# Kernel optimization log

Measured on AMD Instinct MI355X. Metric: run time of the kernel, lower is better.

The kernel has to match this reference:

```python
import jax, jax.numpy as jnp
import numpy as np

NUM_NODES = 100
WINDOW = 128
GH = 256       # graph_hidden_channels
DH = 64        # discrepancy_hidden_channels
OUT = 128      # out_channels
B = 256        # graphs per batch
N = B * NUM_NODES
E = 409600


def _mconv(x, w, b):
    # x: [B, n, W], w: [n, 2, k], b: [n, 2]  (per-node Conv1d(1,2,k), 'same' padding)
    k = w.shape[-1]
    W = x.shape[-1]
    p = k // 2
    xp = jnp.pad(x, ((0, 0), (0, 0), (p, p)))
    win = jnp.stack([xp[..., j:j + W] for j in range(k)], axis=-1)  # [B,n,W,k]
    return jnp.einsum('bnwk,nck->bncw', win, w) + b[None, :, :, None]


def _gcn(x, edge_index, Wg, bg):
    # PyG GCNConv: add self-loops, symmetric normalization, then linear
    Nn = x.shape[0]
    xw = x @ Wg.T
    loops = jnp.arange(Nn, dtype=edge_index.dtype)
    src = jnp.concatenate([edge_index[0], loops])
    dst = jnp.concatenate([edge_index[1], loops])
    deg = jax.ops.segment_sum(jnp.ones(src.shape[0], dtype=xw.dtype), dst, num_segments=Nn)
    norm = jax.lax.rsqrt(jnp.maximum(deg, 1e-12))
    coef = norm[src] * norm[dst]
    agg = jax.ops.segment_sum(coef[:, None] * xw[src], dst, num_segments=Nn)
    return agg + bg


def setup_inputs() -> dict:
    key = jax.random.key(0)
    ks = jax.random.split(key, 20)
    f = 6 * WINDOW
    s = lambda d: 1.0 / np.sqrt(d)
    inp = {
        'x1': jax.random.normal(ks[0], (N, WINDOW), jnp.float32),
        'x2': jax.random.normal(ks[1], (N, WINDOW), jnp.float32),
        'edge_index1': jax.random.randint(ks[2], (2, E), 0, N, jnp.int32),
        'edge_index2': jax.random.randint(ks[3], (2, E), 0, N, jnp.int32),
        'w3': jax.random.normal(ks[4], (NUM_NODES, 2, 3), jnp.float32) * s(3),
        'b3': jax.random.normal(ks[5], (NUM_NODES, 2), jnp.float32) * s(3),
        'w5': jax.random.normal(ks[6], (NUM_NODES, 2, 5), jnp.float32) * s(5),
        'b5': jax.random.normal(ks[7], (NUM_NODES, 2), jnp.float32) * s(5),
        'w7': jax.random.normal(ks[8], (NUM_NODES, 2, 7), jnp.float32) * s(7),
        'b7': jax.random.normal(ks[9], (NUM_NODES, 2), jnp.float32) * s(7),
        'Wff': jax.random.normal(ks[10], (NUM_NODES, GH, f), jnp.float32) * s(f),
        'bff': jax.random.normal(ks[11], (NUM_NODES, GH), jnp.float32) * s(f),
        'Wg': jax.random.normal(ks[12], (GH, GH), jnp.float32) * s(GH),
        'bg': jax.random.normal(ks[13], (GH,), jnp.float32) * s(GH),
        'Wd': jax.random.normal(ks[14], (NUM_NODES, DH, 2 * GH), jnp.float32) * s(2 * GH),
        'bd': jax.random.normal(ks[15], (NUM_NODES, DH), jnp.float32) * s(2 * GH),
        'Wfc': jax.random.normal(ks[16], (OUT, NUM_NODES * DH), jnp.float32) * s(NUM_NODES * DH),
        'bfc': jax.random.normal(ks[17], (OUT,), jnp.float32) * s(NUM_NODES * DH),
    }
    return inp


def reference(x1, x2, edge_index1, edge_index2, w3, b3, w5, b5, w7, b7,
              Wff, bff, Wg, bg, Wd, bd, Wfc, bfc):
    n = w3.shape[0]
    Nn, W = x1.shape
    Bg = Nn // n

    def branch(x):
        xg = x.reshape(Bg, n, W)
        # multiscale CNN: concat conv3/conv5/conv7 along channel -> [B,n,6,W]
        c = jnp.concatenate([_mconv(xg, w3, b3), _mconv(xg, w5, b5), _mconv(xg, w7, b7)], axis=2)
        c = jax.nn.relu(c.reshape(Bg, n, 6 * W))            # channel-major flatten (matches view(-1))
        h = jax.nn.relu(jnp.einsum('bnf,nhf->bnh', c, Wff) + bff)
        return h.reshape(Nn, -1)

    h1 = jax.nn.relu(_gcn(branch(x1), edge_index1, Wg, bg))
    h2 = jax.nn.relu(_gcn(branch(x2), edge_index2, Wg, bg))
    H = h1.shape[-1]
    cat = jnp.concatenate([h1.reshape(Bg, n, H), h2.reshape(Bg, n, H)], axis=-1)  # [B,n,2H]
    d = jnp.einsum('bnf,ndf->bnd', cat, Wd) + bd            # per-node discrepancy FC
    du = jax.nn.relu(d.reshape(Bg, -1))                     # node-major -> [B, n*DH]
    return du @ Wfc.T + bfc
```

## Files before the change

kernel.cpp:

```cpp
#include <hip/hip_runtime.h>

#define DI __device__ __forceinline__

typedef __bf16 bf16_t;
typedef bf16_t bf16x8 __attribute__((ext_vector_type(8)));
typedef float f32x4 __attribute__((ext_vector_type(4)));
typedef ushort ushort8v __attribute__((ext_vector_type(8)));

static constexpr int NNODE = 100, WIN = 128, GH = 256, DH = 64, OUTC = 128, NB = 256;
static constexpr int NTOT = NB * NNODE;
static constexpr int NE = 409600;
static constexpr int FFK = 6 * WIN;
static constexpr size_t CB = (size_t)NNODE * NB * FFK;
static constexpr size_t HB = (size_t)NTOT * GH;
static constexpr int CVT_BLKS = 23264;
static constexpr int NSEG = 64, SEGE = NE / NSEG;
static constexpr int NPK = NTOT / 2;
static constexpr int NRANGE = 4, RDST = NTOT / NRANGE;
static constexpr int RPK = RDST / 2;
static constexpr int HIST_BLKS = 2 * NSEG * NRANGE;

DI ushort f2bf(float f) {
  union { float f; unsigned u; } v; v.f = f;
  unsigned r = v.u + 0x7fffu + ((v.u >> 16) & 1u);
  return (ushort)(r >> 16);
}
DI float bf2f(ushort s) {
  union { unsigned u; float f; } v; v.u = ((unsigned)s) << 16; return v.f;
}
DI float u2f(uint u) { union { uint u; float f; } v; v.u = u; return v.f; }

DI void gload16(const void* g, void* l) {
  __builtin_amdgcn_global_load_lds((const __attribute__((address_space(1))) void*)g,
                                   (__attribute__((address_space(3))) void*)l, 16, 0, 0);
}


DI void cvt_body(int bx, const float* s0, const float* s1, const float* s2, const float* s3,
                 ushort* d0, ushort* d1, ushort* d2, ushort* d3) {
  int j = bx * 256 + threadIdx.x;
  const float* s; ushort* d;
  if (j < 19660800 / 4) { s = s0; d = d0; }
  else if ((j -= 19660800 / 4) < 3276800 / 4) { s = s1; d = d1; }
  else if ((j -= 3276800 / 4) < 819200 / 4) { s = s2; d = d2; }
  else { j -= 819200 / 4; s = s3; d = d3; }
  float4 v = reinterpret_cast<const float4*>(s)[j];
  ushort4 o;
  o.x = f2bf(v.x); o.y = f2bf(v.y); o.z = f2bf(v.z); o.w = f2bf(v.w);
  reinterpret_cast<ushort4*>(d)[j] = o;
}

DI void histseg_body(int bx, const int* e1d, const int* e2d,
                     ushort* rank_local, uint* segcnt, uint* cnt ) {
  int set = bx & 1, seg = (bx >> 1) & (NSEG - 1), range = bx >> 7;
  int tid = threadIdx.x;
  for (int k = tid; k < RPK; k += 256) cnt[k] = 0;
  __syncthreads();
  const int* dstp = (set ? e2d : e1d) + seg * SEGE;
  ushort* rl = rank_local + set * NE + seg * SEGE;
  const int dbase = range * RDST;
#pragma unroll
  for (int k = 0; k < SEGE / 256; ++k) {
    int i = k * 256 + tid;
    uint dl = (uint)(dstp[i] - dbase);
    if (dl < (uint)RDST) {
      uint sh = (dl & 1) * 16;
      uint old = atomicAdd(&cnt[dl >> 1], 1u << sh);
      rl[i] = (ushort)((old >> sh) & 0xffffu);
    }
  }
  __syncthreads();
  uint* sc = segcnt + (size_t)(set * NSEG + seg) * NPK + range * RPK;
  for (int k = tid; k < RPK; k += 256) sc[k] = cnt[k];
}

DI void fill_body(int bx, const int* e1, const int* e2, const int* offs,
                  const ushort* rank_local, const uint* segbase, int* csr) {
  int i = bx * 256 + threadIdx.x;
  int set = i >= NE;
  int ii = i - set * NE;
  const int* e = set ? e2 : e1;
  int d = e[NE + ii];
  int seg = ii / SEGE;
  uint b32 = segbase[(size_t)(set * NSEG + seg) * NPK + (d >> 1)];
  int base = (b32 >> ((d & 1) * 16)) & 0xffff;
  int pos = offs[set * (NTOT + 1) + d] + base + rank_local[i];
  csr[set * NE + pos] = e[ii];
}

DI void segscan_body(int set, int pb, const uint* segcnt, uint* segbase, int* deg) {
  int p = pb * 256 + threadIdx.x;
  uint lo = 0, hi = 0;
  const uint* sc = segcnt + (size_t)set * NSEG * NPK + p;
  uint* sb = segbase + (size_t)set * NSEG * NPK + p;
  for (int s = 0; s < NSEG; ++s) {
    uint v = sc[(size_t)s * NPK];
    sb[(size_t)s * NPK] = lo | (hi << 16);
    lo += v & 0xffffu; hi += v >> 16;
  }
  reinterpret_cast<int2*>(deg)[set * NPK + p] = make_int2((int)lo, (int)hi);
}

DI void scan_body(int set, const int* deg_, int* offs_, float* norm_) {
  const int* deg = deg_ + set * NTOT;
  int* offs = offs_ + set * (NTOT + 1);
  float* norm = norm_ + set * NTOT;
  __shared__ int part[256];
  int t = threadIdx.x;
  int base = t * 100;
  int s = 0;
  for (int j = 0; j < 100; ++j) s += deg[base + j];
  part[t] = s;
  __syncthreads();
  for (int d = 1; d < 256; d <<= 1) {
    int vv = (t >= d) ? part[t - d] : 0;
    __syncthreads();
    part[t] += vv;
    __syncthreads();
  }
  int run = (t > 0) ? part[t - 1] : 0;
  for (int j = 0; j < 100; ++j) {
    int dv = deg[base + j];
    offs[base + j] = run;
    norm[base + j] = rsqrtf((float)(dv + 1));
    run += dv;
  }
  if (t == 255) offs[NTOT] = part[255];
}

DI void conv_body(int bx, const float* x1, const float* x2,
                  const float* w3, const float* b3, const float* w5, const float* b5,
                  const float* w7, const float* b7, ushort* c, float* xs ) {
  const int t = threadIdx.x;
  const int rowi = t >> 4;
  const int idx = t & 15;
  int r = bx * 16 + rowi;
  int br = r >= NTOT;
  int rr = r - br * NTOT;
  const float* x = br ? x2 : x1;
  int b = rr / 100, node = rr - b * 100;

  float* row = xs + rowi * 136;
  const int w0 = idx * 8;
  float4 v0 = *reinterpret_cast<const float4*>(x + (size_t)rr * WIN + w0);
  float4 v1 = *reinterpret_cast<const float4*>(x + (size_t)rr * WIN + w0 + 4);
  *reinterpret_cast<float4*>(&row[4 + w0]) = v0;
  *reinterpret_cast<float4*>(&row[4 + w0 + 4]) = v1;
  if (idx == 0) { row[0] = 0.f; row[1] = 0.f; row[2] = 0.f; row[3] = 0.f; }
  if (idx == 15) { row[132] = 0.f; row[133] = 0.f; row[134] = 0.f; row[135] = 0.f; }
  __syncthreads();

  float xv[14];
#pragma unroll
  for (int j = 0; j < 14; ++j) xv[j] = row[1 + w0 + j];

  const float* W3 = w3 + node * 6;  const float* B3 = b3 + node * 2;
  const float* W5 = w5 + node * 10; const float* B5 = b5 + node * 2;
  const float* W7 = w7 + node * 14; const float* B7 = b7 + node * 2;
  ushort* out = c + (size_t)br * CB + (size_t)(node * NB + b) * FFK + w0;

#pragma unroll
  for (int ch = 0; ch < 2; ++ch) {
    float k3[3], k5[5], k7[7];
#pragma unroll
    for (int j = 0; j < 3; ++j) k3[j] = W3[ch * 3 + j];
#pragma unroll
    for (int j = 0; j < 5; ++j) k5[j] = W5[ch * 5 + j];
#pragma unroll
    for (int j = 0; j < 7; ++j) k7[j] = W7[ch * 7 + j];
    float bb3 = B3[ch], bb5 = B5[ch], bb7 = B7[ch];
    ushort8v o3, o5, o7;
#pragma unroll
    for (int p = 0; p < 8; ++p) {
      float a3 = bb3, a5 = bb5, a7 = bb7;
#pragma unroll
      for (int j = 0; j < 3; ++j) a3 += k3[j] * xv[p + 2 + j];
#pragma unroll
      for (int j = 0; j < 5; ++j) a5 += k5[j] * xv[p + 1 + j];
#pragma unroll
      for (int j = 0; j < 7; ++j) a7 += k7[j] * xv[p + j];
      o3[p] = f2bf(fmaxf(a3, 0.f));
      o5[p] = f2bf(fmaxf(a5, 0.f));
      o7[p] = f2bf(fmaxf(a7, 0.f));
    }
    *reinterpret_cast<ushort8v*>(out + (0 + ch) * WIN) = o3;
    *reinterpret_cast<ushort8v*>(out + (2 + ch) * WIN) = o5;
    *reinterpret_cast<ushort8v*>(out + (4 + ch) * WIN) = o7;
  }
}

template <int MODE>
DI void gemm_body(int bx, int by, const ushort* __restrict__ A, const ushort* __restrict__ A2,
                  const ushort* __restrict__ Bm, ushort* __restrict__ obf,
                  float* __restrict__ of, const float* __restrict__ bias) {
  constexpr int BN = (MODE == 2 || MODE == 0) ? 64 : 128;
  constexpr int KT = (MODE == 0) ? 12 : (MODE == 1) ? 4 : (MODE == 2) ? 8 : 4;
  constexpr int LDA = (MODE == 0) ? 768 : (MODE == 1) ? 256 : (MODE == 2) ? 256 : 6400;
  constexpr int LDB = (MODE == 0) ? 768 : (MODE == 1) ? 256 : (MODE == 2) ? 512 : 6400;
  constexpr int MF = (MODE == 2) ? 2 : 4;
  constexpr int NF = (MODE == 0) ? 2 : 4;
  constexpr int NTW = (MODE == 0) ? 64 : 128;

  __shared__ ushort As[128 * 64];
  __shared__ ushort Bs[BN * 64];

  const int tid = threadIdx.x, wv = tid >> 6, lane = tid & 63;
  const int j8 = (((lane & 7) ^ (lane >> 3)) - (lane & 7)) * 8;

  int mt = 0, nt = 0, node = 0, kbase = 0, br = 0;
  if constexpr (MODE == 0) {
    int h = bx;
    int s = (h & 7) * 200 + (h >> 3);
    nt = s & 3; int rest = s >> 2;
    mt = rest & 1; int yy = rest >> 1;
    br = yy >= 100; node = yy - br * 100;
  } else if constexpr (MODE == 1) {
    int h = bx;
    int s = (h & 7) * 100 + (h >> 3);
    nt = s & 1; int rest = s >> 1;
    br = rest >= 200; mt = rest - br * 200;
  } else if constexpr (MODE == 2) { mt = bx; node = by; }
  else { mt = bx; kbase = by * 256; }

  const ushort* Ab = nullptr; const ushort* Bb = nullptr;
  if constexpr (MODE == 0) { Ab = A + (size_t)br * CB + (size_t)node * (NB * FFK) + (size_t)mt * 128 * FFK;
                             Bb = Bm + (size_t)node * (GH * FFK) + (size_t)nt * 64 * FFK; }
  else if constexpr (MODE == 1) { Ab = A + (size_t)br * HB + (size_t)mt * 128 * GH;
                                  Bb = Bm + (size_t)nt * 128 * GH; }
  else if constexpr (MODE == 2) { Bb = Bm + (size_t)node * (DH * 512); }
  else { Ab = A + (size_t)mt * 128 * 6400 + kbase; Bb = Bm + kbase; }

  const int wr = (MODE == 2) ? wv : (wv >> 1);
  const int wc = (MODE == 2) ? 0 : (wv & 1);

  f32x4 acc[MF][NF] = {};

  for (int kt = 0; kt < KT; ++kt) {
    const int k0 = kt * 64;
    __syncthreads();
#pragma unroll
    for (int it = 0; it < 4; ++it) {
      int rb = it * 32 + wv * 8;
      int row = rb + (lane >> 3);
      const ushort* gp;
      if constexpr (MODE == 2) {
        int b_ = mt * 128 + row;
        const ushort* src = (k0 < 256) ? A : A2;
        gp = src + (size_t)(b_ * NNODE + node) * GH + (k0 & 255) + (lane & 7) * 8 + j8;
      } else {
        gp = Ab + (size_t)row * LDA + k0 + (lane & 7) * 8 + j8;
      }
      gload16(gp, &As[rb * 64]);
    }
#pragma unroll
    for (int it = 0; it < BN / 32; ++it) {
      int rb = it * 32 + wv * 8;
      int row = rb + (lane >> 3);
      gload16(Bb + (size_t)row * LDB + k0 + (lane & 7) * 8 + j8, &Bs[rb * 64]);
    }
    __syncthreads();
#pragma unroll
    for (int kk = 0; kk < 2; ++kk) {
      const int ch8 = ((kk * 4 + (lane >> 4)) ^ (lane & 7)) * 8;
      bf16x8 af[MF], bfr[NF];
#pragma unroll
      for (int m = 0; m < MF; ++m) {
        int rr = wr * (MF * 16) + m * 16 + (lane & 15);
        af[m] = *reinterpret_cast<const bf16x8*>(&As[rr * 64 + ch8]);
      }
#pragma unroll
      for (int n = 0; n < NF; ++n) {
        int rr = wc * (NF * 16) + n * 16 + (lane & 15);
        bfr[n] = *reinterpret_cast<const bf16x8*>(&Bs[rr * 64 + ch8]);
      }
#pragma unroll
      for (int m = 0; m < MF; ++m)
#pragma unroll
        for (int n = 0; n < NF; ++n)
          acc[m][n] = __builtin_amdgcn_mfma_f32_16x16x32_bf16(af[m], bfr[n], acc[m][n], 0, 0, 0);
    }
  }

  const int lrow = (lane >> 4) * 4, lcol = lane & 15;
#pragma unroll
  for (int m = 0; m < MF; ++m) {
#pragma unroll
    for (int n = 0; n < NF; ++n) {
      int cc = wc * (NF * 16) + n * 16 + lcol;
#pragma unroll
      for (int rg = 0; rg < 4; ++rg) {
        int rr = wr * (MF * 16) + m * 16 + lrow + rg;
        float val = acc[m][n][rg];
        if constexpr (MODE == 0) {
          int b_ = mt * 128 + rr;
          int col = nt * NTW + cc;
          val = fmaxf(val + bias[node * GH + col], 0.f);
          obf[(size_t)br * HB + (size_t)(b_ * NNODE + node) * GH + col] = f2bf(val);
        } else if constexpr (MODE == 1) {
          int R = mt * 128 + rr;
          int col = nt * 128 + cc;
          obf[(size_t)br * HB + (size_t)R * GH + col] = f2bf(val * bias[br * NTOT + R]);
        } else if constexpr (MODE == 2) {
          int b_ = mt * 128 + rr;
          val = fmaxf(val + bias[node * DH + cc], 0.f);
          obf[(size_t)b_ * (NNODE * DH) + node * DH + cc] = f2bf(val);
        } else {
          int R = mt * 128 + rr;
          if (by == 0) val += bias[cc];
          atomicAdd(&of[R * OUTC + cc], val);
        }
      }
    }
  }
}


__global__ __launch_bounds__(256) void fused1_k(
    const float* __restrict__ Wff, const float* __restrict__ Wd,
    const float* __restrict__ Wfc, const float* __restrict__ Wg,
    ushort* __restrict__ Wffb, ushort* __restrict__ Wdb,
    ushort* __restrict__ Wfcb, ushort* __restrict__ Wgb,
    const int* __restrict__ e1d, const int* __restrict__ e2d,
    ushort* __restrict__ rank_local, uint* __restrict__ segcnt,
    const float* __restrict__ x1, const float* __restrict__ x2,
    const float* __restrict__ w3, const float* __restrict__ b3,
    const float* __restrict__ w5, const float* __restrict__ b5,
    const float* __restrict__ w7, const float* __restrict__ b7,
    ushort* __restrict__ c) {
  __shared__ uint smem[RPK];
  int bx = blockIdx.x;
  if (bx < HIST_BLKS) histseg_body(bx, e1d, e2d, rank_local, segcnt, smem);
  else if (bx < HIST_BLKS + 3200) conv_body(bx - HIST_BLKS, x1, x2, w3, b3, w5, b5, w7, b7, c, (float*)smem);
  else cvt_body(bx - HIST_BLKS - 3200, Wff, Wd, Wfc, Wg, Wffb, Wdb, Wfcb, Wgb);
}

__global__ __launch_bounds__(256) void fused3_k(
    const ushort* __restrict__ cbuf, const ushort* __restrict__ Wffb,
    ushort* __restrict__ h, const float* __restrict__ bff,
    const uint* __restrict__ segcnt, uint* __restrict__ segbase, int* __restrict__ deg) {
  if ((int)blockIdx.x < 1600)
    gemm_body<0>(blockIdx.x, 0, cbuf, nullptr, Wffb, h, nullptr, bff);
  else {
    int b = blockIdx.x - 1600;
    segscan_body(b / 50, b % 50, segcnt, segbase, deg);
  }
}

__global__ __launch_bounds__(256) void scan_k(const int* __restrict__ deg,
                                              int* __restrict__ offs, float* __restrict__ nrm) {
  scan_body(blockIdx.x, deg, offs, nrm);
}

__global__ __launch_bounds__(256) void fused4_k(
    const ushort* __restrict__ h, const ushort* __restrict__ Wgb,
    ushort* __restrict__ xw, const float* __restrict__ nrm,
    const int* __restrict__ e1, const int* __restrict__ e2,
    const int* __restrict__ offs, const ushort* __restrict__ rank_local,
    const uint* __restrict__ segbase, int* __restrict__ csr) {
  if ((int)blockIdx.x < 800)
    gemm_body<1>(blockIdx.x, 0, h, nullptr, Wgb, xw, nullptr, nrm);
  else
    fill_body(blockIdx.x - 800, e1, e2, offs, rank_local, segbase, csr);
}

template <int MODE>
__global__ __launch_bounds__(256) void gemm_k(const ushort* __restrict__ A, const ushort* __restrict__ A2,
                                              const ushort* __restrict__ Bm, ushort* __restrict__ obf,
                                              float* __restrict__ of, const float* __restrict__ bias) {
  gemm_body<MODE>(blockIdx.x, blockIdx.y, A, A2, Bm, obf, of, bias);
}

__global__ __launch_bounds__(256) void agg_k(const ushort* __restrict__ xw_, const int* __restrict__ offs_,
                                             const int* __restrict__ csr_, const float* __restrict__ norm_,
                                             const float* __restrict__ bg, ushort* __restrict__ hg_) {
  int bid = blockIdx.x;
  int c = bid & 7;
  int i = bid >> 3;
  int br = c >> 2, slice = c & 3;
  int g = threadIdx.x >> 3;
  int v = i * 32 + g;
  int l8 = threadIdx.x & 7;
  int col = slice * 64 + l8 * 8;

  const ushort* xw = xw_ + (size_t)br * HB;
  const int* offs = offs_ + br * (NTOT + 1);
  const int* csr = csr_ + br * NE;
  const float* norm = norm_ + br * NTOT;
  ushort* hg = hg_ + (size_t)br * HB;
  const uint* base = reinterpret_cast<const uint*>(xw + col);

  float a[8];
  {
    uint4 q = *reinterpret_cast<const uint4*>(base + (size_t)v * (GH / 2));
    a[0] = u2f(q.x << 16); a[1] = u2f(q.x & 0xffff0000u);
    a[2] = u2f(q.y << 16); a[3] = u2f(q.y & 0xffff0000u);
    a[4] = u2f(q.z << 16); a[5] = u2f(q.z & 0xffff0000u);
    a[6] = u2f(q.w << 16); a[7] = u2f(q.w & 0xffff0000u);
  }
  int e0 = offs[v], e1v = offs[v + 1];
  int j = e0;
  for (; j + 1 < e1v; j += 2) {
    int s0 = csr[j], s1 = csr[j + 1];
    uint4 q0 = *reinterpret_cast<const uint4*>(base + (size_t)s0 * (GH / 2));
    uint4 q1 = *reinterpret_cast<const uint4*>(base + (size_t)s1 * (GH / 2));
    a[0] += u2f(q0.x << 16) + u2f(q1.x << 16);
    a[1] += u2f(q0.x & 0xffff0000u) + u2f(q1.x & 0xffff0000u);
    a[2] += u2f(q0.y << 16) + u2f(q1.y << 16);
    a[3] += u2f(q0.y & 0xffff0000u) + u2f(q1.y & 0xffff0000u);
    a[4] += u2f(q0.z << 16) + u2f(q1.z << 16);
    a[5] += u2f(q0.z & 0xffff0000u) + u2f(q1.z & 0xffff0000u);
    a[6] += u2f(q0.w << 16) + u2f(q1.w << 16);
    a[7] += u2f(q0.w & 0xffff0000u) + u2f(q1.w & 0xffff0000u);
  }
  if (j < e1v) {
    int s0 = csr[j];
    uint4 q0 = *reinterpret_cast<const uint4*>(base + (size_t)s0 * (GH / 2));
    a[0] += u2f(q0.x << 16); a[1] += u2f(q0.x & 0xffff0000u);
    a[2] += u2f(q0.y << 16); a[3] += u2f(q0.y & 0xffff0000u);
    a[4] += u2f(q0.z << 16); a[5] += u2f(q0.z & 0xffff0000u);
    a[6] += u2f(q0.w << 16); a[7] += u2f(q0.w & 0xffff0000u);
  }

  float nv = norm[v];
  float4 bb0 = *reinterpret_cast<const float4*>(bg + col);
  float4 bb1 = *reinterpret_cast<const float4*>(bg + col + 4);
  ushort8v o;
  o[0] = f2bf(fmaxf(nv * a[0] + bb0.x, 0.f));
  o[1] = f2bf(fmaxf(nv * a[1] + bb0.y, 0.f));
  o[2] = f2bf(fmaxf(nv * a[2] + bb0.z, 0.f));
  o[3] = f2bf(fmaxf(nv * a[3] + bb0.w, 0.f));
  o[4] = f2bf(fmaxf(nv * a[4] + bb1.x, 0.f));
  o[5] = f2bf(fmaxf(nv * a[5] + bb1.y, 0.f));
  o[6] = f2bf(fmaxf(nv * a[6] + bb1.z, 0.f));
  o[7] = f2bf(fmaxf(nv * a[7] + bb1.w, 0.f));
  *reinterpret_cast<ushort8v*>(hg + (size_t)v * GH + col) = o;
}

extern "C" void kernel_launch(void* const* d_in, const int* in_sizes, int n_in,
                              void* d_out, int out_size, void* d_ws, size_t ws_size,
                              hipStream_t stream) {
  const float* x1 = (const float*)d_in[0];
  const float* x2 = (const float*)d_in[1];
  const int* e1 = (const int*)d_in[2];
  const int* e2 = (const int*)d_in[3];
  const float* w3 = (const float*)d_in[4];  const float* b3 = (const float*)d_in[5];
  const float* w5 = (const float*)d_in[6];  const float* b5 = (const float*)d_in[7];
  const float* w7 = (const float*)d_in[8];  const float* b7 = (const float*)d_in[9];
  const float* Wff = (const float*)d_in[10]; const float* bff = (const float*)d_in[11];
  const float* Wg = (const float*)d_in[12];  const float* bg = (const float*)d_in[13];
  const float* Wd = (const float*)d_in[14];  const float* bd = (const float*)d_in[15];
  const float* Wfc = (const float*)d_in[16]; const float* bfc = (const float*)d_in[17];
  float* out = (float*)d_out;

  char* ws = (char*)d_ws;
  size_t off = 0;
  auto alloc = [&](size_t bytes) -> char* {
    char* p = ws + off;
    off = (off + bytes + 255) & ~(size_t)255;
    return p;
  };
  ushort* Wffb = (ushort*)alloc(19660800ull * 2);
  ushort* Wdb  = (ushort*)alloc(3276800ull * 2);
  ushort* Wfcb = (ushort*)alloc(819200ull * 2);
  ushort* Wgb  = (ushort*)alloc(65536ull * 2);
  ushort* cbuf = (ushort*)alloc(2 * CB * 2);
  ushort* h    = (ushort*)alloc(2 * HB * 2);
  ushort* xw   = (ushort*)alloc(2 * HB * 2);
  int* deg     = (int*)alloc(2 * NTOT * 4);
  int* offs    = (int*)alloc(2 * (NTOT + 1) * 4);
  ushort* rankl = (ushort*)alloc(2 * NE * 2);
  uint* segcnt  = (uint*)alloc((size_t)2 * NSEG * NPK * 4);
  uint* segbase = (uint*)alloc((size_t)2 * NSEG * NPK * 4);
  int* csr     = (int*)alloc(2 * NE * 4);
  float* nrm   = (float*)alloc(2 * NTOT * 4);
  ushort* du = cbuf;

  hipMemsetAsync(out, 0, (size_t)out_size * 4, stream);

  fused1_k<<<HIST_BLKS + 3200 + CVT_BLKS, 256, 0, stream>>>(
      Wff, Wd, Wfc, Wg, Wffb, Wdb, Wfcb, Wgb,
      e1 + NE, e2 + NE, rankl, segcnt,
      x1, x2, w3, b3, w5, b5, w7, b7, cbuf);
  fused3_k<<<1700, 256, 0, stream>>>(cbuf, Wffb, h, bff, segcnt, segbase, deg);
  scan_k<<<2, 256, 0, stream>>>(deg, offs, nrm);
  fused4_k<<<4000, 256, 0, stream>>>(h, Wgb, xw, nrm, e1, e2, offs, rankl, segbase, csr);

  agg_k<<<6400, 256, 0, stream>>>(xw, offs, csr, nrm, bg, h);

  gemm_k<2><<<dim3(2, 100), 256, 0, stream>>>(h, h + HB, Wdb, du, nullptr, bd);
  gemm_k<3><<<dim3(2, 25), 256, 0, stream>>>(du, nullptr, Wfcb, nullptr, out, bfc);
}
```

Before: 229.2 us.

## Fuse multiscale conv into per-node FF GEMM, computing A tiles on the fly

The multiscale Conv1d is no longer a separate pass that writes a large bf16 intermediate buffer. Each FF GEMM block now loads the raw input rows into registers and builds the conv+ReLU A-tile directly in shared memory for each K chunk. This removes a global write and read of the conv activations and one stage of fused1, but the conv is recomputed by every N-tile block (four per node/m-tile), and the scalar input loads are uncoalesced and bounds-checked.

```diff
diff --git a/kernel.cpp b/kernel.cpp
--- a/kernel.cpp
+++ b/kernel.cpp
@@ -11,7 +11,6 @@
 static constexpr int NTOT = NB * NNODE;
 static constexpr int NE = 409600;
 static constexpr int FFK = 6 * WIN;
-static constexpr size_t CB = (size_t)NNODE * NB * FFK;
 static constexpr size_t HB = (size_t)NTOT * GH;
 static constexpr int CVT_BLKS = 23264;
 static constexpr int NSEG = 64, SEGE = NE / NSEG;
@@ -128,64 +127,116 @@
   if (t == 255) offs[NTOT] = part[255];
 }
 
-DI void conv_body(int bx, const float* x1, const float* x2,
-                  const float* w3, const float* b3, const float* w5, const float* b5,
-                  const float* w7, const float* b7, ushort* c, float* xs ) {
-  const int t = threadIdx.x;
-  const int rowi = t >> 4;
-  const int idx = t & 15;
-  int r = bx * 16 + rowi;
-  int br = r >= NTOT;
-  int rr = r - br * NTOT;
+DI void gemm0f_body(int bx,
+                    const float* __restrict__ x1, const float* __restrict__ x2,
+                    const float* __restrict__ w3, const float* __restrict__ b3,
+                    const float* __restrict__ w5, const float* __restrict__ b5,
+                    const float* __restrict__ w7, const float* __restrict__ b7,
+                    const ushort* __restrict__ Wffb, ushort* __restrict__ h,
+                    const float* __restrict__ bff) {
+  __shared__ ushort As[128 * 64];
+  __shared__ ushort Bs[64 * 64];
+
+  const int tid = threadIdx.x, wv = tid >> 6, lane = tid & 63;
+  const int j8 = (((lane & 7) ^ (lane >> 3)) - (lane & 7)) * 8;
+
+  int s = (bx & 7) * 200 + (bx >> 3);
+  int nt = s & 3; int rest = s >> 2;
+  int mt = rest & 1; int yy = rest >> 1;
+  int br = yy >= 100; int node = yy - br * 100;
+
   const float* x = br ? x2 : x1;
-  int b = rr / 100, node = rr - b * 100;
-
-  float* row = xs + rowi * 136;
-  const int w0 = idx * 8;
-  float4 v0 = *reinterpret_cast<const float4*>(x + (size_t)rr * WIN + w0);
-  float4 v1 = *reinterpret_cast<const float4*>(x + (size_t)rr * WIN + w0 + 4);
-  *reinterpret_cast<float4*>(&row[4 + w0]) = v0;
-  *reinterpret_cast<float4*>(&row[4 + w0 + 4]) = v1;
-  if (idx == 0) { row[0] = 0.f; row[1] = 0.f; row[2] = 0.f; row[3] = 0.f; }
-  if (idx == 15) { row[132] = 0.f; row[133] = 0.f; row[134] = 0.f; row[135] = 0.f; }
-  __syncthreads();
-
-  float xv[14];
-#pragma unroll
-  for (int j = 0; j < 14; ++j) xv[j] = row[1 + w0 + j];
-
-  const float* W3 = w3 + node * 6;  const float* B3 = b3 + node * 2;
-  const float* W5 = w5 + node * 10; const float* B5 = b5 + node * 2;
-  const float* W7 = w7 + node * 14; const float* B7 = b7 + node * 2;
-  ushort* out = c + (size_t)br * CB + (size_t)(node * NB + b) * FFK + w0;
-
-#pragma unroll
-  for (int ch = 0; ch < 2; ++ch) {
-    float k3[3], k5[5], k7[7];
-#pragma unroll
-    for (int j = 0; j < 3; ++j) k3[j] = W3[ch * 3 + j];
-#pragma unroll
-    for (int j = 0; j < 5; ++j) k5[j] = W5[ch * 5 + j];
-#pragma unroll
-    for (int j = 0; j < 7; ++j) k7[j] = W7[ch * 7 + j];
-    float bb3 = B3[ch], bb5 = B5[ch], bb7 = B7[ch];
-    ushort8v o3, o5, o7;
-#pragma unroll
-    for (int p = 0; p < 8; ++p) {
-      float a3 = bb3, a5 = bb5, a7 = bb7;
-#pragma unroll
-      for (int j = 0; j < 3; ++j) a3 += k3[j] * xv[p + 2 + j];
-#pragma unroll
-      for (int j = 0; j < 5; ++j) a5 += k5[j] * xv[p + 1 + j];
-#pragma unroll
-      for (int j = 0; j < 7; ++j) a7 += k7[j] * xv[p + j];
-      o3[p] = f2bf(fmaxf(a3, 0.f));
-      o5[p] = f2bf(fmaxf(a5, 0.f));
-      o7[p] = f2bf(fmaxf(a7, 0.f));
-    }
-    *reinterpret_cast<ushort8v*>(out + (0 + ch) * WIN) = o3;
-    *reinterpret_cast<ushort8v*>(out + (2 + ch) * WIN) = o5;
-    *reinterpret_cast<ushort8v*>(out + (4 + ch) * WIN) = o7;
+  const ushort* Bb = Wffb + (size_t)node * (GH * FFK) + (size_t)nt * 64 * FFK;
+
+  const int cc = tid & 7;
+  const int rg = tid >> 3;
+  const int wr = wv >> 1, wc = wv & 1;
+
+  f32x4 acc[4][2] = {};
+
+  for (int ph = 0; ph < 2; ++ph) {
+    const int w0 = ph * 64;
+    float xv[4][14];
+    const int sbase = w0 + cc * 8 - 3;
+#pragma unroll
+    for (int rj = 0; rj < 4; ++rj) {
+      const float* xp = x + (size_t)((mt * 128 + rg * 4 + rj) * NNODE + node) * WIN;
+#pragma unroll
+      for (int j = 0; j < 14; ++j) {
+        int idx = sbase + j;
+        xv[rj][j] = (idx >= 0 && idx < WIN) ? xp[idx] : 0.f;
+      }
+    }
+#pragma unroll
+    for (int c6 = 0; c6 < 6; ++c6) {
+      const int kt = c6 * 2 + ph;
+      const int k0 = kt * 64;
+      const int L = (c6 < 2) ? 3 : (c6 < 4) ? 5 : 7;
+      const int off = 3 - L / 2;
+      const float* W = (c6 < 2) ? (w3 + node * 6 + (c6 & 1) * 3)
+                     : (c6 < 4) ? (w5 + node * 10 + (c6 & 1) * 5)
+                                : (w7 + node * 14 + (c6 & 1) * 7);
+      const float kb = ((c6 < 2) ? b3 : (c6 < 4) ? b5 : b7)[node * 2 + (c6 & 1)];
+
+      __syncthreads();
+#pragma unroll
+      for (int it = 0; it < 2; ++it) {
+        int rb = it * 32 + wv * 8;
+        int row = rb + (lane >> 3);
+        gload16(Bb + (size_t)row * FFK + k0 + (lane & 7) * 8 + j8, &Bs[rb * 64]);
+      }
+#pragma unroll
+      for (int rj = 0; rj < 4; ++rj) {
+        int r = rg * 4 + rj;
+        ushort8v o;
+#pragma unroll
+        for (int p = 0; p < 8; ++p) {
+          float a = kb;
+#pragma unroll
+          for (int q = 0; q < 7; ++q)
+            if (q < L) a += W[q] * xv[rj][p + off + q];
+          o[p] = f2bf(fmaxf(a, 0.f));
+        }
+        *reinterpret_cast<ushort8v*>(&As[r * 64 + ((cc ^ (r & 7)) * 8)]) = o;
+      }
+      __syncthreads();
+#pragma unroll
+      for (int kk = 0; kk < 2; ++kk) {
+        const int ch8 = ((kk * 4 + (lane >> 4)) ^ (lane & 7)) * 8;
+        bf16x8 af[4], bfr[2];
+#pragma unroll
+        for (int m = 0; m < 4; ++m) {
+          int rr = wr * 64 + m * 16 + (lane & 15);
+          af[m] = *reinterpret_cast<const bf16x8*>(&As[rr * 64 + ch8]);
+        }
+#pragma unroll
+        for (int n = 0; n < 2; ++n) {
+          int rr = wc * 32 + n * 16 + (lane & 15);
+          bfr[n] = *reinterpret_cast<const bf16x8*>(&Bs[rr * 64 + ch8]);
+        }
+#pragma unroll
+        for (int m = 0; m < 4; ++m)
+#pragma unroll
+          for (int n = 0; n < 2; ++n)
+            acc[m][n] = __builtin_amdgcn_mfma_f32_16x16x32_bf16(af[m], bfr[n], acc[m][n], 0, 0, 0);
+      }
+    }
+  }
+
+  const int lrow = (lane >> 4) * 4, lcol = lane & 15;
+#pragma unroll
+  for (int m = 0; m < 4; ++m) {
+#pragma unroll
+    for (int n = 0; n < 2; ++n) {
+      int col = nt * 64 + wc * 32 + n * 16 + lcol;
+#pragma unroll
+      for (int rg2 = 0; rg2 < 4; ++rg2) {
+        int rr = wr * 64 + m * 16 + lrow + rg2;
+        int b_ = mt * 128 + rr;
+        float val = fmaxf(acc[m][n][rg2] + bff[node * GH + col], 0.f);
+        h[(size_t)br * HB + (size_t)(b_ * NNODE + node) * GH + col] = f2bf(val);
+      }
+    }
   }
 }
 
@@ -193,13 +244,12 @@
 DI void gemm_body(int bx, int by, const ushort* __restrict__ A, const ushort* __restrict__ A2,
                   const ushort* __restrict__ Bm, ushort* __restrict__ obf,
                   float* __restrict__ of, const float* __restrict__ bias) {
-  constexpr int BN = (MODE == 2 || MODE == 0) ? 64 : 128;
-  constexpr int KT = (MODE == 0) ? 12 : (MODE == 1) ? 4 : (MODE == 2) ? 8 : 4;
-  constexpr int LDA = (MODE == 0) ? 768 : (MODE == 1) ? 256 : (MODE == 2) ? 256 : 6400;
-  constexpr int LDB = (MODE == 0) ? 768 : (MODE == 1) ? 256 : (MODE == 2) ? 512 : 6400;
+  constexpr int BN = (MODE == 2) ? 64 : 128;
+  constexpr int KT = (MODE == 1) ? 4 : (MODE == 2) ? 8 : 4;
+  constexpr int LDA = (MODE == 1) ? 256 : (MODE == 2) ? 256 : 6400;
+  constexpr int LDB = (MODE == 1) ? 256 : (MODE == 2) ? 512 : 6400;
   constexpr int MF = (MODE == 2) ? 2 : 4;
-  constexpr int NF = (MODE == 0) ? 2 : 4;
-  constexpr int NTW = (MODE == 0) ? 64 : 128;
+  constexpr int NF = 4;
 
   __shared__ ushort As[128 * 64];
   __shared__ ushort Bs[BN * 64];
@@ -208,13 +258,7 @@
   const int j8 = (((lane & 7) ^ (lane >> 3)) - (lane & 7)) * 8;
 
   int mt = 0, nt = 0, node = 0, kbase = 0, br = 0;
-  if constexpr (MODE == 0) {
-    int h = bx;
-    int s = (h & 7) * 200 + (h >> 3);
-    nt = s & 3; int rest = s >> 2;
-    mt = rest & 1; int yy = rest >> 1;
-    br = yy >= 100; node = yy - br * 100;
-  } else if constexpr (MODE == 1) {
+  if constexpr (MODE == 1) {
     int h = bx;
     int s = (h & 7) * 100 + (h >> 3);
     nt = s & 1; int rest = s >> 1;
@@ -223,10 +267,8 @@
   else { mt = bx; kbase = by * 256; }
 
   const ushort* Ab = nullptr; const ushort* Bb = nullptr;
-  if constexpr (MODE == 0) { Ab = A + (size_t)br * CB + (size_t)node * (NB * FFK) + (size_t)mt * 128 * FFK;
-                             Bb = Bm + (size_t)node * (GH * FFK) + (size_t)nt * 64 * FFK; }
-  else if constexpr (MODE == 1) { Ab = A + (size_t)br * HB + (size_t)mt * 128 * GH;
-                                  Bb = Bm + (size_t)nt * 128 * GH; }
+  if constexpr (MODE == 1) { Ab = A + (size_t)br * HB + (size_t)mt * 128 * GH;
+                             Bb = Bm + (size_t)nt * 128 * GH; }
   else if constexpr (MODE == 2) { Bb = Bm + (size_t)node * (DH * 512); }
   else { Ab = A + (size_t)mt * 128 * 6400 + kbase; Bb = Bm + kbase; }
 
@@ -291,12 +333,7 @@
       for (int rg = 0; rg < 4; ++rg) {
         int rr = wr * (MF * 16) + m * 16 + lrow + rg;
         float val = acc[m][n][rg];
-        if constexpr (MODE == 0) {
-          int b_ = mt * 128 + rr;
-          int col = nt * NTW + cc;
-          val = fmaxf(val + bias[node * GH + col], 0.f);
-          obf[(size_t)br * HB + (size_t)(b_ * NNODE + node) * GH + col] = f2bf(val);
-        } else if constexpr (MODE == 1) {
+        if constexpr (MODE == 1) {
           int R = mt * 128 + rr;
           int col = nt * 128 + cc;
           obf[(size_t)br * HB + (size_t)R * GH + col] = f2bf(val * bias[br * NTOT + R]);
@@ -321,25 +358,22 @@
     ushort* __restrict__ Wffb, ushort* __restrict__ Wdb,
     ushort* __restrict__ Wfcb, ushort* __restrict__ Wgb,
     const int* __restrict__ e1d, const int* __restrict__ e2d,
-    ushort* __restrict__ rank_local, uint* __restrict__ segcnt,
+    ushort* __restrict__ rank_local, uint* __restrict__ segcnt) {
+  __shared__ uint smem[RPK];
+  int bx = blockIdx.x;
+  if (bx < HIST_BLKS) histseg_body(bx, e1d, e2d, rank_local, segcnt, smem);
+  else cvt_body(bx - HIST_BLKS, Wff, Wd, Wfc, Wg, Wffb, Wdb, Wfcb, Wgb);
+}
+
+__global__ __launch_bounds__(256) void fused3_k(
     const float* __restrict__ x1, const float* __restrict__ x2,
     const float* __restrict__ w3, const float* __restrict__ b3,
     const float* __restrict__ w5, const float* __restrict__ b5,
     const float* __restrict__ w7, const float* __restrict__ b7,
-    ushort* __restrict__ c) {
-  __shared__ uint smem[RPK];
-  int bx = blockIdx.x;
-  if (bx < HIST_BLKS) histseg_body(bx, e1d, e2d, rank_local, segcnt, smem);
-  else if (bx < HIST_BLKS + 3200) conv_body(bx - HIST_BLKS, x1, x2, w3, b3, w5, b5, w7, b7, c, (float*)smem);
-  else cvt_body(bx - HIST_BLKS - 3200, Wff, Wd, Wfc, Wg, Wffb, Wdb, Wfcb, Wgb);
-}
-
-__global__ __launch_bounds__(256) void fused3_k(
-    const ushort* __restrict__ cbuf, const ushort* __restrict__ Wffb,
-    ushort* __restrict__ h, const float* __restrict__ bff,
+    const ushort* __restrict__ Wffb, ushort* __restrict__ h, const float* __restrict__ bff,
     const uint* __restrict__ segcnt, uint* __restrict__ segbase, int* __restrict__ deg) {
   if ((int)blockIdx.x < 1600)
-    gemm_body<0>(blockIdx.x, 0, cbuf, nullptr, Wffb, h, nullptr, bff);
+    gemm0f_body(blockIdx.x, x1, x2, w3, b3, w5, b5, w7, b7, Wffb, h, bff);
   else {
     int b = blockIdx.x - 1600;
     segscan_body(b / 50, b % 50, segcnt, segbase, deg);
@@ -463,9 +497,9 @@
   ushort* Wdb  = (ushort*)alloc(3276800ull * 2);
   ushort* Wfcb = (ushort*)alloc(819200ull * 2);
   ushort* Wgb  = (ushort*)alloc(65536ull * 2);
-  ushort* cbuf = (ushort*)alloc(2 * CB * 2);
   ushort* h    = (ushort*)alloc(2 * HB * 2);
   ushort* xw   = (ushort*)alloc(2 * HB * 2);
+  ushort* du   = (ushort*)alloc((size_t)NB * NNODE * DH * 2);
   int* deg     = (int*)alloc(2 * NTOT * 4);
   int* offs    = (int*)alloc(2 * (NTOT + 1) * 4);
   ushort* rankl = (ushort*)alloc(2 * NE * 2);
@@ -473,15 +507,14 @@
   uint* segbase = (uint*)alloc((size_t)2 * NSEG * NPK * 4);
   int* csr     = (int*)alloc(2 * NE * 4);
   float* nrm   = (float*)alloc(2 * NTOT * 4);
-  ushort* du = cbuf;
 
   hipMemsetAsync(out, 0, (size_t)out_size * 4, stream);
 
-  fused1_k<<<HIST_BLKS + 3200 + CVT_BLKS, 256, 0, stream>>>(
+  fused1_k<<<HIST_BLKS + CVT_BLKS, 256, 0, stream>>>(
       Wff, Wd, Wfc, Wg, Wffb, Wdb, Wfcb, Wgb,
-      e1 + NE, e2 + NE, rankl, segcnt,
-      x1, x2, w3, b3, w5, b5, w7, b7, cbuf);
-  fused3_k<<<1700, 256, 0, stream>>>(cbuf, Wffb, h, bff, segcnt, segbase, deg);
+      e1 + NE, e2 + NE, rankl, segcnt);
+  fused3_k<<<1700, 256, 0, stream>>>(x1, x2, w3, b3, w5, b5, w7, b7,
+                                     Wffb, h, bff, segcnt, segbase, deg);
   scan_k<<<2, 256, 0, stream>>>(deg, offs, nrm);
   fused4_k<<<4000, 256, 0, stream>>>(h, Wgb, xw, nrm, e1, e2, offs, rankl, segbase, csr);
 
```

Result: slower. 269.2 us (+17.4%).
